# Performance work log

Measured on AMD Instinct MI355X. Metric: run time of the kernel, lower is better.

Reference implementation:

```python
import jax, jax.numpy as jnp
import numpy as np

NEG = -1.0e9


def setup_inputs() -> dict:
    key = jax.random.key(0)
    ks = jax.random.split(key, 8)
    B, L, D = 4, 2048, 1024
    s = 1.0 / np.sqrt(D)
    return {
        "x": jax.random.normal(ks[0], (B, L, D), dtype=jnp.float32),
        "Wq": jax.random.normal(ks[1], (D, D), dtype=jnp.float32) * s,
        "bq": jax.random.normal(ks[2], (D,), dtype=jnp.float32) * 0.02,
        "Wk": jax.random.normal(ks[3], (D, D), dtype=jnp.float32) * s,
        "bk": jax.random.normal(ks[4], (D,), dtype=jnp.float32) * 0.02,
        "Wv": jax.random.normal(ks[5], (D, D), dtype=jnp.float32) * s,
        "bv": jax.random.normal(ks[6], (D,), dtype=jnp.float32) * 0.02,
        "lengths": jax.random.randint(ks[7], (B,), 1, 2048, dtype=jnp.int32),
    }


def reference(x, Wq, bq, Wk, bk, Wv, bv, lengths):
    # x: [B, L, D]; single-head self-attention with causal + length additive masks
    B, L, D = x.shape
    q = x @ Wq + bq  # [B, L, D]
    k = x @ Wk + bk
    v = x @ Wv + bv
    scale = 1.0 / jnp.sqrt(jnp.asarray(D, dtype=x.dtype))
    att = jnp.einsum("bid,bjd->bij", q, k) * scale  # [B, L, L]
    idx = jnp.arange(L)
    causal = jnp.where(idx[None, :] > idx[:, None], NEG, 0.0).astype(x.dtype)  # [L, L]
    # length mask: NEG where j >= len[b] or i >= len[b]
    invalid = (idx[None, :] >= lengths[:, None])  # [B, L]
    lenmask = jnp.where(invalid[:, :, None] | invalid[:, None, :], NEG, 0.0).astype(x.dtype)
    att = att + causal[None, :, :] + lenmask
    att = jax.nn.softmax(att, axis=-1)
    return jnp.einsum("bij,bjd->bid", att, v)
```

## Files before the change

### kernel.cpp

```cpp
#include <hip/hip_runtime.h>

#define NEGV (-1.0e9f)

typedef __bf16 bf16_t;
typedef __bf16 bf16x8 __attribute__((ext_vector_type(8)));
typedef __bf16 bf16x4 __attribute__((ext_vector_type(4)));
typedef float  f32x4  __attribute__((ext_vector_type(4)));

__device__ __forceinline__ void gld16(const void* g, void* l) {
    __builtin_amdgcn_global_load_lds(
        (const __attribute__((address_space(1))) void*)g,
        (__attribute__((address_space(3))) void*)l, 16, 0, 0);
}


#define MMR(AF, IB)                                                                        \
    acc[IB][0] = __builtin_amdgcn_mfma_f32_16x16x32_bf16(AF, b0, acc[IB][0], 0, 0, 0);     \
    acc[IB][1] = __builtin_amdgcn_mfma_f32_16x16x32_bf16(AF, b1, acc[IB][1], 0, 0, 0);     \
    acc[IB][2] = __builtin_amdgcn_mfma_f32_16x16x32_bf16(AF, b2, acc[IB][2], 0, 0, 0);     \
    acc[IB][3] = __builtin_amdgcn_mfma_f32_16x16x32_bf16(AF, b3, acc[IB][3], 0, 0, 0)

__device__ __forceinline__ void ml256x256(
    const bf16_t* __restrict__ A, const bf16_t* __restrict__ B,
    int ldA, int ldB, int nkt, char* smem, int tid, f32x4 acc[8][4])
{
    const int w = tid >> 6, lane = tid & 63;
    const int wm = w & 1, wn = w >> 1;
    const int l16 = lane & 15, quad = lane >> 4;

    const int g0 = 2 * (tid >> 3) + ((tid >> 2) & 1);
    const int c0 = ((tid & 3) ^ ((tid >> 3) & 3)) * 8;
    const bf16_t* pa0 = A + (size_t)g0 * ldA + c0;
    const bf16_t* pa1 = pa0 + (size_t)128 * ldA;
    const bf16_t* pb0 = B + (size_t)g0 * ldB + c0;
    const bf16_t* pb1 = pb0 + (size_t)128 * ldB;
    char* const stA = smem + (w << 10);
    char* const stB = smem + 16384 + (w << 10);

    const int rowo = (l16 >> 1) * 128 + (l16 & 1) * 64 + ((quad ^ ((l16 >> 1) & 3)) << 4);
    const char* rdA = smem + (wm << 13) + rowo;
    const char* rdB = smem + 16384 + (wn << 12) + rowo;

#define STG6(BO) do { gld16(pa0, stA + (BO)); gld16(pa1, stA + (BO) + 8192);   \
                      gld16(pb0, stB + (BO)); gld16(pb1, stB + (BO) + 8192);   \
                      pa0 += 32; pa1 += 32; pb0 += 32; pb1 += 32; } while (0)

    STG6(0);
    if (nkt > 1) {
        STG6(32768);
        asm volatile("s_waitcnt vmcnt(4)" ::: "memory");
    } else {
        asm volatile("s_waitcnt vmcnt(0)" ::: "memory");
    }
    __builtin_amdgcn_s_barrier();

    int ro = 0, so = 65536;
    for (int kt = 0; kt < nkt; ++kt) {
        const char* ra = rdA + ro;
        const char* rb = rdB + ro;
        bf16x8 a0 = *(const bf16x8*)(ra);
        bf16x8 a1 = *(const bf16x8*)(ra + 1024);
        bf16x8 a2 = *(const bf16x8*)(ra + 2048);
        bf16x8 a3 = *(const bf16x8*)(ra + 3072);
        bf16x8 b0 = *(const bf16x8*)(rb);
        bf16x8 b1 = *(const bf16x8*)(rb + 1024);
        bf16x8 b2 = *(const bf16x8*)(rb + 2048);
        bf16x8 b3 = *(const bf16x8*)(rb + 3072);
        bf16x8 a4 = *(const bf16x8*)(ra + 4096);
        bf16x8 a5 = *(const bf16x8*)(ra + 5120);
        bf16x8 a6 = *(const bf16x8*)(ra + 6144);
        bf16x8 a7 = *(const bf16x8*)(ra + 7168);
        const bool st = (kt + 2) < nkt;
        if (st) STG6(so);
        asm volatile("s_waitcnt lgkmcnt(4)" ::: "memory");
        __builtin_amdgcn_sched_barrier(0);
        __builtin_amdgcn_s_setprio(1);
        MMR(a0, 0); MMR(a1, 1); MMR(a2, 2); MMR(a3, 3);
        __builtin_amdgcn_s_setprio(0);
        asm volatile("s_waitcnt lgkmcnt(0)" ::: "memory");
        __builtin_amdgcn_sched_barrier(0);
        __builtin_amdgcn_s_setprio(1);
        MMR(a4, 4); MMR(a5, 5); MMR(a6, 6); MMR(a7, 7);
        __builtin_amdgcn_s_setprio(0);
        if (st) asm volatile("s_waitcnt vmcnt(4)" ::: "memory");
        else    asm volatile("s_waitcnt vmcnt(0)" ::: "memory");
        __builtin_amdgcn_s_barrier();
        ro = (ro == 65536) ? 0 : (ro + 32768);
        so = (so == 65536) ? 0 : (so + 32768);
    }
#undef STG6
}

__device__ __forceinline__ void ml256x128(
    const bf16_t* __restrict__ A, const bf16_t* __restrict__ B,
    int ldA, int ldB, int nkt, char* smem, int tid, f32x4 acc[4][4])
{
    const int w = tid >> 6, lane = tid & 63;
    const int wm = w & 3, wn = w >> 2;
    const int l16 = lane & 15, quad = lane >> 4;

    const int g0 = 2 * (tid >> 3) + ((tid >> 2) & 1);
    const int c0 = ((tid & 3) ^ ((tid >> 3) & 3)) * 8;
    const bf16_t* pa0 = A + (size_t)g0 * ldA + c0;
    const bf16_t* pa1 = pa0 + (size_t)128 * ldA;
    const bf16_t* pb0 = B + (size_t)g0 * ldB + c0;
    char* const stA = smem + (w << 10);
    char* const stB = smem + 16384 + (w << 10);

    const int rowo = (l16 >> 1) * 128 + (l16 & 1) * 64 + ((quad ^ ((l16 >> 1) & 3)) << 4);
    const char* rdA = smem + (wm << 12) + rowo;
    const char* rdB = smem + 16384 + (wn << 12) + rowo;

#define STG3(BO) do { gld16(pa0, stA + (BO)); gld16(pa1, stA + (BO) + 8192);   \
                      gld16(pb0, stB + (BO));                                  \
                      pa0 += 32; pa1 += 32; pb0 += 32; } while (0)

    STG3(0);
    if (nkt > 1) {
        STG3(24576);
        asm volatile("s_waitcnt vmcnt(3)" ::: "memory");
    } else {
        asm volatile("s_waitcnt vmcnt(0)" ::: "memory");
    }
    __builtin_amdgcn_s_barrier();

    int ro = 0, so = 49152;
    for (int kt = 0; kt < nkt; ++kt) {
        const char* ra = rdA + ro;
        const char* rb = rdB + ro;
        bf16x8 a0 = *(const bf16x8*)(ra);
        bf16x8 a1 = *(const bf16x8*)(ra + 1024);
        bf16x8 a2 = *(const bf16x8*)(ra + 2048);
        bf16x8 a3 = *(const bf16x8*)(ra + 3072);
        bf16x8 b0 = *(const bf16x8*)(rb);
        bf16x8 b1 = *(const bf16x8*)(rb + 1024);
        bf16x8 b2 = *(const bf16x8*)(rb + 2048);
        bf16x8 b3 = *(const bf16x8*)(rb + 3072);
        const bool st = (kt + 2) < nkt;
        if (st) STG3(so);
        asm volatile("s_waitcnt lgkmcnt(0)" ::: "memory");
        __builtin_amdgcn_sched_barrier(0);
        __builtin_amdgcn_s_setprio(1);
        MMR(a0, 0); MMR(a1, 1); MMR(a2, 2); MMR(a3, 3);
        __builtin_amdgcn_s_setprio(0);
        if (st) asm volatile("s_waitcnt vmcnt(3)" ::: "memory");
        else    asm volatile("s_waitcnt vmcnt(0)" ::: "memory");
        __builtin_amdgcn_s_barrier();
        ro = (ro == 49152) ? 0 : (ro + 24576);
        so = (so == 49152) ? 0 : (so + 24576);
    }
#undef STG3
}

__global__ __launch_bounds__(256)
void convert_x_kernel(const float* __restrict__ x, bf16_t* __restrict__ xb)
{
    const size_t i = ((size_t)blockIdx.x * 256 + threadIdx.x) * 8;
    float4 a = *(const float4*)&x[i];
    float4 b = *(const float4*)&x[i + 4];
    bf16x8 o;
    o[0] = (bf16_t)a.x; o[1] = (bf16_t)a.y; o[2] = (bf16_t)a.z; o[3] = (bf16_t)a.w;
    o[4] = (bf16_t)b.x; o[5] = (bf16_t)b.y; o[6] = (bf16_t)b.z; o[7] = (bf16_t)b.w;
    *(bf16x8*)&xb[i] = o;
}

__global__ __launch_bounds__(256)
void transpose_w_kernel(const float* __restrict__ W0, const float* __restrict__ W1,
                        const float* __restrict__ W2, bf16_t* __restrict__ WT)
{
    __shared__ float t[32][33];
    const float* W = (blockIdx.z == 0) ? W0 : (blockIdx.z == 1) ? W1 : W2;
    bf16_t* WTz = WT + (size_t)blockIdx.z * 1024 * 1024;
    const int k0 = blockIdx.y * 32, n0 = blockIdx.x * 32;
    const int r = threadIdx.x >> 3, c4 = (threadIdx.x & 7) * 4;
    float4 v = *(const float4*)&W[(size_t)(k0 + r) * 1024 + n0 + c4];
    t[r][c4 + 0] = v.x; t[r][c4 + 1] = v.y; t[r][c4 + 2] = v.z; t[r][c4 + 3] = v.w;
    __syncthreads();
    bf16x4 o;
#pragma unroll
    for (int j = 0; j < 4; ++j) o[j] = (bf16_t)t[c4 + j][r];
    *(bf16x4*)&WTz[(size_t)(n0 + r) * 1024 + k0 + c4] = o;
}

__global__ __launch_bounds__(512, 2)
void gemm_qk256(const bf16_t* __restrict__ A, const bf16_t* __restrict__ Bt,
                const float* __restrict__ bq, const float* __restrict__ bk,
                bf16_t* __restrict__ C, int N, int Kd)
{
    __shared__ __align__(16) char smem[98304];
    int bid = blockIdx.y * 8 + blockIdx.x;
    bid = (bid & 7) * 32 + (bid >> 3);
    const int n0 = (bid & 7) * 256;
    const int m0 = (bid >> 3) * 256;
    const int tid = threadIdx.x;

    f32x4 acc[8][4];
#pragma unroll
    for (int i = 0; i < 8; ++i)
#pragma unroll
        for (int j = 0; j < 4; ++j) acc[i][j] = (f32x4)(0.0f);

    ml256x256(A + (size_t)m0 * Kd, Bt + (size_t)n0 * Kd, Kd, Kd, Kd >> 5,
              smem, tid, acc);

    const int w = tid >> 6, lane = tid & 63;
    const int wm = w & 1, wn = w >> 1, quad = lane >> 4, l16 = lane & 15;
#pragma unroll
    for (int j = 0; j < 4; ++j) {
        const int col = n0 + wn * 64 + j * 16 + l16;
        const float bval = (col < 1024) ? bq[col] : bk[col - 1024];
#pragma unroll
        for (int i = 0; i < 8; ++i) {
            const int row = m0 + wm * 128 + i * 16 + quad * 4;
#pragma unroll
            for (int r = 0; r < 4; ++r)
                C[(size_t)(row + r) * N + col] = (bf16_t)(acc[i][j][r] + bval);
        }
    }
}

__global__ __launch_bounds__(512, 2)
void gemm_vt256(const bf16_t* __restrict__ WvT, const bf16_t* __restrict__ xb,
                const float* __restrict__ bv, bf16_t* __restrict__ VT,
                int N, int Kd)
{
    __shared__ __align__(16) char smem[73728];
    int bid = blockIdx.y * 64 + blockIdx.x;
    bid = (bid & 7) * 32 + (bid >> 3);
    const int m0 = (bid >> 6) * 256;
    const int n0 = (bid & 63) * 128;
    const int tid = threadIdx.x;

    f32x4 acc[4][4];
#pragma unroll
    for (int i = 0; i < 4; ++i)
#pragma unroll
        for (int j = 0; j < 4; ++j) acc[i][j] = (f32x4)(0.0f);

    ml256x128(WvT + (size_t)m0 * Kd, xb + (size_t)n0 * Kd, Kd, Kd, Kd >> 5,
              smem, tid, acc);

    const int w = tid >> 6, lane = tid & 63;
    const int wm = w & 3, wn = w >> 2, quad = lane >> 4, l16 = lane & 15;
#pragma unroll
    for (int i = 0; i < 4; ++i) {
        const int row = m0 + wm * 64 + i * 16 + quad * 4;
#pragma unroll
        for (int r = 0; r < 4; ++r) {
            const float bval = bv[row + r];
#pragma unroll
            for (int j = 0; j < 4; ++j) {
                const int col = n0 + wn * 64 + j * 16 + l16;
                VT[(size_t)(row + r) * N + col] = (bf16_t)(acc[i][j][r] + bval);
            }
        }
    }
}

__global__ __launch_bounds__(512, 2)
void scores256(const bf16_t* __restrict__ Q, const bf16_t* __restrict__ K,
               int ldq, const int* __restrict__ lengths,
               bf16_t* __restrict__ U, float2* __restrict__ stats,
               int L, int Dd, float alpha)
{
    __shared__ __align__(16) char smem[98304];
    const int b = blockIdx.z;
    const int len = lengths[b];
    int it = 0;
    while ((it + 1) * (it + 2) / 2 <= (int)blockIdx.x) ++it;
    const int jt = blockIdx.x - it * (it + 1) / 2;
    const int m0 = it * 256, n0 = jt * 256;
    const int tid = threadIdx.x;

    f32x4 acc[8][4];
#pragma unroll
    for (int i = 0; i < 8; ++i)
#pragma unroll
        for (int j = 0; j < 4; ++j) acc[i][j] = (f32x4)(0.0f);

    const bf16_t* Qb = Q + (size_t)b * L * ldq + (size_t)m0 * ldq;
    const bf16_t* Kb = K + (size_t)b * L * ldq + (size_t)n0 * ldq;
    ml256x256(Qb, Kb, ldq, ldq, Dd >> 5, smem, tid, acc);

    const int w = tid >> 6, lane = tid & 63;
    const int wm = w & 1, wn = w >> 1, quad = lane >> 4, l16 = lane & 15;
    bf16_t* Ub = U + (size_t)b * L * L;
    float2* strow = stats + (size_t)b * L * 32;
    const int chnk = (n0 >> 6) + wn;
#pragma unroll
    for (int i = 0; i < 8; ++i) {
#pragma unroll
        for (int r = 0; r < 4; ++r) {
            const int row = m0 + wm * 128 + i * 16 + quad * 4 + r;
            float sv[4];
#pragma unroll
            for (int j = 0; j < 4; ++j) {
                const int col = n0 + wn * 64 + j * 16 + l16;
                float v = acc[i][j][r] * alpha;
                if (col > row) v += NEGV;
                if (row >= len || col >= len) v += NEGV;
                sv[j] = v;
            }
            float m = fmaxf(fmaxf(sv[0], sv[1]), fmaxf(sv[2], sv[3]));
            m = fmaxf(m, __shfl_xor(m, 1, 64));
            m = fmaxf(m, __shfl_xor(m, 2, 64));
            m = fmaxf(m, __shfl_xor(m, 4, 64));
            m = fmaxf(m, __shfl_xor(m, 8, 64));
            float ssum = 0.f;
#pragma unroll
            for (int j = 0; j < 4; ++j) {
                sv[j] = __expf(sv[j] - m);
                ssum += sv[j];
            }
            ssum += __shfl_xor(ssum, 1, 64);
            ssum += __shfl_xor(ssum, 2, 64);
            ssum += __shfl_xor(ssum, 4, 64);
            ssum += __shfl_xor(ssum, 8, 64);
#pragma unroll
            for (int j = 0; j < 4; ++j)
                Ub[(size_t)row * L + n0 + wn * 64 + j * 16 + l16] = (bf16_t)sv[j];
            if (l16 == 0) strow[(size_t)row * 32 + chnk] = make_float2(m, ssum);
        }
    }
}

__global__ __launch_bounds__(256)
void sm_finalize_norm(const float2* __restrict__ stats, bf16_t* __restrict__ U,
                      int L)
{
    __shared__ float sc[32];
    const int i = blockIdx.x;
    const int bound2 = ((i >> 8) + 1) << 8;
    const int nch = bound2 >> 6;
    const size_t base = ((size_t)blockIdx.y * L + i) * 32;
    const int t = threadIdx.x;

    if (t < 32) {
        float m_c = -3.0e38f, s_c = 0.f;
        if (t < nch) { float2 st = stats[base + t]; m_c = st.x; s_c = st.y; }
        float M = m_c;
        M = fmaxf(M, __shfl_xor(M, 1, 64));
        M = fmaxf(M, __shfl_xor(M, 2, 64));
        M = fmaxf(M, __shfl_xor(M, 4, 64));
        M = fmaxf(M, __shfl_xor(M, 8, 64));
        M = fmaxf(M, __shfl_xor(M, 16, 64));
        const float e = __expf(m_c - M);
        float d = s_c * e;
        d += __shfl_xor(d, 1, 64);
        d += __shfl_xor(d, 2, 64);
        d += __shfl_xor(d, 4, 64);
        d += __shfl_xor(d, 8, 64);
        d += __shfl_xor(d, 16, 64);
        sc[t] = e / d;
    }
    __syncthreads();

    const int j8 = t * 8;
    if (j8 < bound2) {
        bf16_t* row = U + ((size_t)blockIdx.y * L + i) * L;
        bf16x8 u = *(const bf16x8*)&row[j8];
        const float c = sc[t >> 3];
        bf16x8 o;
#pragma unroll
        for (int j = 0; j < 8; ++j) o[j] = (bf16_t)((float)u[j] * c);
        *(bf16x8*)&row[j8] = o;
    }
}

__global__ __launch_bounds__(512, 2)
void pv256(const bf16_t* __restrict__ P, int ldp,
           const bf16_t* __restrict__ VT, int ldv,
           float* __restrict__ O, int L, int Dd)
{
    __shared__ __align__(16) char smem[73728];
    const int b = blockIdx.z;
    int bid = blockIdx.y * 8 + blockIdx.x;
    bid = (bid & 7) * 8 + (bid >> 3);
    const int mt = 7 - (bid >> 3);
    const int m0 = mt * 256, n0 = (bid & 7) * 128;
    const int tid = threadIdx.x;

    f32x4 acc[4][4];
#pragma unroll
    for (int i = 0; i < 4; ++i)
#pragma unroll
        for (int j = 0; j < 4; ++j) acc[i][j] = (f32x4)(0.0f);

    const int nkt = (m0 + 256) >> 5;
    const bf16_t* Pb = P + (size_t)b * L * ldp + (size_t)m0 * ldp;
    const bf16_t* Vb = VT + (size_t)b * L + (size_t)n0 * ldv;
    ml256x128(Pb, Vb, ldp, ldv, nkt, smem, tid, acc);

    float* Ob = O + (size_t)b * L * Dd;
    const int w = tid >> 6, lane = tid & 63;
    const int wm = w & 3, wn = w >> 2, quad = lane >> 4, l16 = lane & 15;
#pragma unroll
    for (int i = 0; i < 4; ++i) {
        const int row = m0 + wm * 64 + i * 16 + quad * 4;
#pragma unroll
        for (int j = 0; j < 4; ++j) {
            const int col = n0 + wn * 64 + j * 16 + l16;
#pragma unroll
            for (int r = 0; r < 4; ++r)
                Ob[(size_t)(row + r) * Dd + col] = acc[i][j][r];
        }
    }
}

extern "C" void kernel_launch(void* const* d_in, const int* in_sizes, int n_in,
                              void* d_out, int out_size, void* d_ws, size_t ws_size,
                              hipStream_t stream)
{
    const float* x  = (const float*)d_in[0];
    const float* Wq = (const float*)d_in[1];
    const float* bq = (const float*)d_in[2];
    const float* Wk = (const float*)d_in[3];
    const float* bk = (const float*)d_in[4];
    const float* Wv = (const float*)d_in[5];
    const float* bv = (const float*)d_in[6];
    const int*  len = (const int*)d_in[7];
    float* out = (float*)d_out;

    const int B = 4, L = 2048, D = 1024;
    const int M = B * L;
    const int N2 = 2 * D;

    bf16_t* xb = (bf16_t*)d_ws;
    bf16_t* WT = xb + (size_t)M * D;
    bf16_t* QK = WT + (size_t)3 * D * D;
    bf16_t* VT = QK + (size_t)M * N2;
    bf16_t* U  = VT + (size_t)D * M;
    float2* stats = (float2*)(U + (size_t)B * L * L);

    convert_x_kernel<<<(M * D) / 2048, 256, 0, stream>>>(x, xb);

    transpose_w_kernel<<<dim3(32, 32, 3), 256, 0, stream>>>(Wq, Wk, Wv, WT);

    gemm_qk256<<<dim3(8, 32), 512, 0, stream>>>(xb, WT, bq, bk, QK, N2, D);

    gemm_vt256<<<dim3(64, 4), 512, 0, stream>>>(
        WT + (size_t)2 * D * D, xb, bv, VT, M, D);

    scores256<<<dim3(36, 1, B), 512, 0, stream>>>(
        QK, QK + 1024, N2, len, U, stats, L, D, 0.03125f);

    sm_finalize_norm<<<dim3(L, B), 256, 0, stream>>>(stats, U, L);

    pv256<<<dim3(8, 8, 4), 512, 0, stream>>>(U, L, VT, M, out, L, D);
}
```

Before: 246.2 us.

## Switch all GEMM stages to 128x128 tiles with 256-thread blocks

Replaces the 256x256 and 256x128 MFMA mainloops with a single 128x128 tile mainloop using 4 waves. The QK, V-transpose, scores and PV kernels all move to this smaller tile, which raises block counts and gives finer triangular granularity for the causal score and PV work. Tile-index swizzles are adjusted to match, and the normalization bound is tightened to 128-column granularity. Smaller tiles lower data reuse per block and add more global/LDS traffic relative to MFMA work, in exchange for better load balance and occupancy.

```diff
diff --git a/kernel.cpp b/kernel.cpp
--- a/kernel.cpp
+++ b/kernel.cpp
@@ -20,9 +20,9 @@
     acc[IB][2] = __builtin_amdgcn_mfma_f32_16x16x32_bf16(AF, b2, acc[IB][2], 0, 0, 0);     \
     acc[IB][3] = __builtin_amdgcn_mfma_f32_16x16x32_bf16(AF, b3, acc[IB][3], 0, 0, 0)
 
-__device__ __forceinline__ void ml256x256(
+__device__ __forceinline__ void ml128x128(
     const bf16_t* __restrict__ A, const bf16_t* __restrict__ B,
-    int ldA, int ldB, int nkt, char* smem, int tid, f32x4 acc[8][4])
+    int ldA, int ldB, int nkt, char* smem, int tid, f32x4 acc[4][4])
 {
     const int w = tid >> 6, lane = tid & 63;
     const int wm = w & 1, wn = w >> 1;
@@ -31,100 +31,30 @@
     const int g0 = 2 * (tid >> 3) + ((tid >> 2) & 1);
     const int c0 = ((tid & 3) ^ ((tid >> 3) & 3)) * 8;
     const bf16_t* pa0 = A + (size_t)g0 * ldA + c0;
-    const bf16_t* pa1 = pa0 + (size_t)128 * ldA;
+    const bf16_t* pa1 = pa0 + (size_t)64 * ldA;
     const bf16_t* pb0 = B + (size_t)g0 * ldB + c0;
-    const bf16_t* pb1 = pb0 + (size_t)128 * ldB;
+    const bf16_t* pb1 = pb0 + (size_t)64 * ldB;
     char* const stA = smem + (w << 10);
-    char* const stB = smem + 16384 + (w << 10);
+    char* const stB = smem + 24576 + (w << 10);
 
     const int rowo = (l16 >> 1) * 128 + (l16 & 1) * 64 + ((quad ^ ((l16 >> 1) & 3)) << 4);
-    const char* rdA = smem + (wm << 13) + rowo;
-    const char* rdB = smem + 16384 + (wn << 12) + rowo;
-
-#define STG6(BO) do { gld16(pa0, stA + (BO)); gld16(pa1, stA + (BO) + 8192);   \
-                      gld16(pb0, stB + (BO)); gld16(pb1, stB + (BO) + 8192);   \
+    const char* rdA = smem + (wm << 12) + rowo;
+    const char* rdB = smem + 24576 + (wn << 12) + rowo;
+
+#define STG4(BO) do { gld16(pa0, stA + (BO)); gld16(pa1, stA + (BO) + 4096);   \
+                      gld16(pb0, stB + (BO)); gld16(pb1, stB + (BO) + 4096);   \
                       pa0 += 32; pa1 += 32; pb0 += 32; pb1 += 32; } while (0)
 
-    STG6(0);
+    STG4(0);
     if (nkt > 1) {
-        STG6(32768);
+        STG4(8192);
         asm volatile("s_waitcnt vmcnt(4)" ::: "memory");
     } else {
         asm volatile("s_waitcnt vmcnt(0)" ::: "memory");
     }
     __builtin_amdgcn_s_barrier();
 
-    int ro = 0, so = 65536;
-    for (int kt = 0; kt < nkt; ++kt) {
-        const char* ra = rdA + ro;
-        const char* rb = rdB + ro;
-        bf16x8 a0 = *(const bf16x8*)(ra);
-        bf16x8 a1 = *(const bf16x8*)(ra + 1024);
-        bf16x8 a2 = *(const bf16x8*)(ra + 2048);
-        bf16x8 a3 = *(const bf16x8*)(ra + 3072);
-        bf16x8 b0 = *(const bf16x8*)(rb);
-        bf16x8 b1 = *(const bf16x8*)(rb + 1024);
-        bf16x8 b2 = *(const bf16x8*)(rb + 2048);
-        bf16x8 b3 = *(const bf16x8*)(rb + 3072);
-        bf16x8 a4 = *(const bf16x8*)(ra + 4096);
-        bf16x8 a5 = *(const bf16x8*)(ra + 5120);
-        bf16x8 a6 = *(const bf16x8*)(ra + 6144);
-        bf16x8 a7 = *(const bf16x8*)(ra + 7168);
-        const bool st = (kt + 2) < nkt;
-        if (st) STG6(so);
-        asm volatile("s_waitcnt lgkmcnt(4)" ::: "memory");
-        __builtin_amdgcn_sched_barrier(0);
-        __builtin_amdgcn_s_setprio(1);
-        MMR(a0, 0); MMR(a1, 1); MMR(a2, 2); MMR(a3, 3);
-        __builtin_amdgcn_s_setprio(0);
-        asm volatile("s_waitcnt lgkmcnt(0)" ::: "memory");
-        __builtin_amdgcn_sched_barrier(0);
-        __builtin_amdgcn_s_setprio(1);
-        MMR(a4, 4); MMR(a5, 5); MMR(a6, 6); MMR(a7, 7);
-        __builtin_amdgcn_s_setprio(0);
-        if (st) asm volatile("s_waitcnt vmcnt(4)" ::: "memory");
-        else    asm volatile("s_waitcnt vmcnt(0)" ::: "memory");
-        __builtin_amdgcn_s_barrier();
-        ro = (ro == 65536) ? 0 : (ro + 32768);
-        so = (so == 65536) ? 0 : (so + 32768);
-    }
-#undef STG6
-}
-
-__device__ __forceinline__ void ml256x128(
-    const bf16_t* __restrict__ A, const bf16_t* __restrict__ B,
-    int ldA, int ldB, int nkt, char* smem, int tid, f32x4 acc[4][4])
-{
-    const int w = tid >> 6, lane = tid & 63;
-    const int wm = w & 3, wn = w >> 2;
-    const int l16 = lane & 15, quad = lane >> 4;
-
-    const int g0 = 2 * (tid >> 3) + ((tid >> 2) & 1);
-    const int c0 = ((tid & 3) ^ ((tid >> 3) & 3)) * 8;
-    const bf16_t* pa0 = A + (size_t)g0 * ldA + c0;
-    const bf16_t* pa1 = pa0 + (size_t)128 * ldA;
-    const bf16_t* pb0 = B + (size_t)g0 * ldB + c0;
-    char* const stA = smem + (w << 10);
-    char* const stB = smem + 16384 + (w << 10);
-
-    const int rowo = (l16 >> 1) * 128 + (l16 & 1) * 64 + ((quad ^ ((l16 >> 1) & 3)) << 4);
-    const char* rdA = smem + (wm << 12) + rowo;
-    const char* rdB = smem + 16384 + (wn << 12) + rowo;
-
-#define STG3(BO) do { gld16(pa0, stA + (BO)); gld16(pa1, stA + (BO) + 8192);   \
-                      gld16(pb0, stB + (BO));                                  \
-                      pa0 += 32; pa1 += 32; pb0 += 32; } while (0)
-
-    STG3(0);
-    if (nkt > 1) {
-        STG3(24576);
-        asm volatile("s_waitcnt vmcnt(3)" ::: "memory");
-    } else {
-        asm volatile("s_waitcnt vmcnt(0)" ::: "memory");
-    }
-    __builtin_amdgcn_s_barrier();
-
-    int ro = 0, so = 49152;
+    int ro = 0, so = 16384;
     for (int kt = 0; kt < nkt; ++kt) {
         const char* ra = rdA + ro;
         const char* rb = rdB + ro;
@@ -137,19 +67,19 @@
         bf16x8 b2 = *(const bf16x8*)(rb + 2048);
         bf16x8 b3 = *(const bf16x8*)(rb + 3072);
         const bool st = (kt + 2) < nkt;
-        if (st) STG3(so);
+        if (st) STG4(so);
         asm volatile("s_waitcnt lgkmcnt(0)" ::: "memory");
         __builtin_amdgcn_sched_barrier(0);
         __builtin_amdgcn_s_setprio(1);
         MMR(a0, 0); MMR(a1, 1); MMR(a2, 2); MMR(a3, 3);
         __builtin_amdgcn_s_setprio(0);
-        if (st) asm volatile("s_waitcnt vmcnt(3)" ::: "memory");
+        if (st) asm volatile("s_waitcnt vmcnt(4)" ::: "memory");
         else    asm volatile("s_waitcnt vmcnt(0)" ::: "memory");
         __builtin_amdgcn_s_barrier();
-        ro = (ro == 49152) ? 0 : (ro + 24576);
-        so = (so == 49152) ? 0 : (so + 24576);
-    }
-#undef STG3
+        ro = (ro == 16384) ? 0 : (ro + 8192);
+        so = (so == 16384) ? 0 : (so + 8192);
+    }
+#undef STG4
 }
 
 __global__ __launch_bounds__(256)
@@ -182,25 +112,25 @@
     *(bf16x4*)&WTz[(size_t)(n0 + r) * 1024 + k0 + c4] = o;
 }
 
-__global__ __launch_bounds__(512, 2)
-void gemm_qk256(const bf16_t* __restrict__ A, const bf16_t* __restrict__ Bt,
+__global__ __launch_bounds__(256)
+void gemm_qk128(const bf16_t* __restrict__ A, const bf16_t* __restrict__ Bt,
                 const float* __restrict__ bq, const float* __restrict__ bk,
                 bf16_t* __restrict__ C, int N, int Kd)
 {
-    __shared__ __align__(16) char smem[98304];
-    int bid = blockIdx.y * 8 + blockIdx.x;
-    bid = (bid & 7) * 32 + (bid >> 3);
-    const int n0 = (bid & 7) * 256;
-    const int m0 = (bid >> 3) * 256;
+    __shared__ __align__(16) char smem[49152];
+    int bid = blockIdx.y * 16 + blockIdx.x;
+    bid = (bid & 7) * 128 + (bid >> 3);
+    const int n0 = (bid & 15) << 7;
+    const int m0 = (bid >> 4) << 7;
     const int tid = threadIdx.x;
 
-    f32x4 acc[8][4];
-#pragma unroll
-    for (int i = 0; i < 8; ++i)
+    f32x4 acc[4][4];
+#pragma unroll
+    for (int i = 0; i < 4; ++i)
 #pragma unroll
         for (int j = 0; j < 4; ++j) acc[i][j] = (f32x4)(0.0f);
 
-    ml256x256(A + (size_t)m0 * Kd, Bt + (size_t)n0 * Kd, Kd, Kd, Kd >> 5,
+    ml128x128(A + (size_t)m0 * Kd, Bt + (size_t)n0 * Kd, Kd, Kd, Kd >> 5,
               smem, tid, acc);
 
     const int w = tid >> 6, lane = tid & 63;
@@ -210,8 +140,8 @@
         const int col = n0 + wn * 64 + j * 16 + l16;
         const float bval = (col < 1024) ? bq[col] : bk[col - 1024];
 #pragma unroll
-        for (int i = 0; i < 8; ++i) {
-            const int row = m0 + wm * 128 + i * 16 + quad * 4;
+        for (int i = 0; i < 4; ++i) {
+            const int row = m0 + wm * 64 + i * 16 + quad * 4;
 #pragma unroll
             for (int r = 0; r < 4; ++r)
                 C[(size_t)(row + r) * N + col] = (bf16_t)(acc[i][j][r] + bval);
@@ -219,16 +149,16 @@
     }
 }
 
-__global__ __launch_bounds__(512, 2)
-void gemm_vt256(const bf16_t* __restrict__ WvT, const bf16_t* __restrict__ xb,
+__global__ __launch_bounds__(256)
+void gemm_vt128(const bf16_t* __restrict__ WvT, const bf16_t* __restrict__ xb,
                 const float* __restrict__ bv, bf16_t* __restrict__ VT,
                 int N, int Kd)
 {
-    __shared__ __align__(16) char smem[73728];
+    __shared__ __align__(16) char smem[49152];
     int bid = blockIdx.y * 64 + blockIdx.x;
-    bid = (bid & 7) * 32 + (bid >> 3);
-    const int m0 = (bid >> 6) * 256;
-    const int n0 = (bid & 63) * 128;
+    bid = (bid & 7) * 64 + (bid >> 3);
+    const int m0 = (bid >> 6) << 7;
+    const int n0 = (bid & 63) << 7;
     const int tid = threadIdx.x;
 
     f32x4 acc[4][4];
@@ -237,11 +167,11 @@
 #pragma unroll
         for (int j = 0; j < 4; ++j) acc[i][j] = (f32x4)(0.0f);
 
-    ml256x128(WvT + (size_t)m0 * Kd, xb + (size_t)n0 * Kd, Kd, Kd, Kd >> 5,
+    ml128x128(WvT + (size_t)m0 * Kd, xb + (size_t)n0 * Kd, Kd, Kd, Kd >> 5,
               smem, tid, acc);
 
     const int w = tid >> 6, lane = tid & 63;
-    const int wm = w & 3, wn = w >> 2, quad = lane >> 4, l16 = lane & 15;
+    const int wm = w & 1, wn = w >> 1, quad = lane >> 4, l16 = lane & 15;
 #pragma unroll
     for (int i = 0; i < 4; ++i) {
         const int row = m0 + wm * 64 + i * 16 + quad * 4;
@@ -257,30 +187,32 @@
     }
 }
 
-__global__ __launch_bounds__(512, 2)
-void scores256(const bf16_t* __restrict__ Q, const bf16_t* __restrict__ K,
+__global__ __launch_bounds__(256)
+void scores128(const bf16_t* __restrict__ Q, const bf16_t* __restrict__ K,
                int ldq, const int* __restrict__ lengths,
                bf16_t* __restrict__ U, float2* __restrict__ stats,
                int L, int Dd, float alpha)
 {
-    __shared__ __align__(16) char smem[98304];
+    __shared__ __align__(16) char smem[49152];
     const int b = blockIdx.z;
     const int len = lengths[b];
+    int tix = (int)blockIdx.x;
+    tix = (tix & 7) * 17 + (tix >> 3);
     int it = 0;
-    while ((it + 1) * (it + 2) / 2 <= (int)blockIdx.x) ++it;
-    const int jt = blockIdx.x - it * (it + 1) / 2;
-    const int m0 = it * 256, n0 = jt * 256;
+    while ((it + 1) * (it + 2) / 2 <= tix) ++it;
+    const int jt = tix - it * (it + 1) / 2;
+    const int m0 = it << 7, n0 = jt << 7;
     const int tid = threadIdx.x;
 
-    f32x4 acc[8][4];
-#pragma unroll
-    for (int i = 0; i < 8; ++i)
+    f32x4 acc[4][4];
+#pragma unroll
+    for (int i = 0; i < 4; ++i)
 #pragma unroll
         for (int j = 0; j < 4; ++j) acc[i][j] = (f32x4)(0.0f);
 
     const bf16_t* Qb = Q + (size_t)b * L * ldq + (size_t)m0 * ldq;
     const bf16_t* Kb = K + (size_t)b * L * ldq + (size_t)n0 * ldq;
-    ml256x256(Qb, Kb, ldq, ldq, Dd >> 5, smem, tid, acc);
+    ml128x128(Qb, Kb, ldq, ldq, Dd >> 5, smem, tid, acc);
 
     const int w = tid >> 6, lane = tid & 63;
     const int wm = w & 1, wn = w >> 1, quad = lane >> 4, l16 = lane & 15;
@@ -288,10 +220,10 @@
     float2* strow = stats + (size_t)b * L * 32;
     const int chnk = (n0 >> 6) + wn;
 #pragma unroll
-    for (int i = 0; i < 8; ++i) {
+    for (int i = 0; i < 4; ++i) {
 #pragma unroll
         for (int r = 0; r < 4; ++r) {
-            const int row = m0 + wm * 128 + i * 16 + quad * 4 + r;
+            const int row = m0 + wm * 64 + i * 16 + quad * 4 + r;
             float sv[4];
 #pragma unroll
             for (int j = 0; j < 4; ++j) {
@@ -330,8 +262,8 @@
 {
     __shared__ float sc[32];
     const int i = blockIdx.x;
-    const int bound2 = ((i >> 8) + 1) << 8;
-    const int nch = bound2 >> 6;
+    const int bound = ((i >> 7) + 1) << 7;
+    const int nch = bound >> 6;
     const size_t base = ((size_t)blockIdx.y * L + i) * 32;
     const int t = threadIdx.x;
 
@@ -356,7 +288,7 @@
     __syncthreads();
 
     const int j8 = t * 8;
-    if (j8 < bound2) {
+    if (j8 < bound) {
         bf16_t* row = U + ((size_t)blockIdx.y * L + i) * L;
         bf16x8 u = *(const bf16x8*)&row[j8];
         const float c = sc[t >> 3];
@@ -367,17 +299,16 @@
     }
 }
 
-__global__ __launch_bounds__(512, 2)
-void pv256(const bf16_t* __restrict__ P, int ldp,
+__global__ __launch_bounds__(256)
+void pv128(const bf16_t* __restrict__ P, int ldp,
            const bf16_t* __restrict__ VT, int ldv,
            float* __restrict__ O, int L, int Dd)
 {
-    __shared__ __align__(16) char smem[73728];
+    __shared__ __align__(16) char smem[49152];
     const int b = blockIdx.z;
-    int bid = blockIdx.y * 8 + blockIdx.x;
-    bid = (bid & 7) * 8 + (bid >> 3);
-    const int mt = 7 - (bid >> 3);
-    const int m0 = mt * 256, n0 = (bid & 7) * 128;
+    const int bid = blockIdx.y * 8 + blockIdx.x;
+    const int mt = 15 - (bid >> 3);
+    const int m0 = mt << 7, n0 = (bid & 7) << 7;
     const int tid = threadIdx.x;
 
     f32x4 acc[4][4];
@@ -386,14 +317,14 @@
 #pragma unroll
         for (int j = 0; j < 4; ++j) acc[i][j] = (f32x4)(0.0f);
 
-    const int nkt = (m0 + 256) >> 5;
+    const int nkt = (m0 + 128) >> 5;
     const bf16_t* Pb = P + (size_t)b * L * ldp + (size_t)m0 * ldp;
     const bf16_t* Vb = VT + (size_t)b * L + (size_t)n0 * ldv;
-    ml256x128(Pb, Vb, ldp, ldv, nkt, smem, tid, acc);
+    ml128x128(Pb, Vb, ldp, ldv, nkt, smem, tid, acc);
 
     float* Ob = O + (size_t)b * L * Dd;
     const int w = tid >> 6, lane = tid & 63;
-    const int wm = w & 3, wn = w >> 2, quad = lane >> 4, l16 = lane & 15;
+    const int wm = w & 1, wn = w >> 1, quad = lane >> 4, l16 = lane & 15;
 #pragma unroll
     for (int i = 0; i < 4; ++i) {
         const int row = m0 + wm * 64 + i * 16 + quad * 4;
@@ -436,15 +367,15 @@
 
     transpose_w_kernel<<<dim3(32, 32, 3), 256, 0, stream>>>(Wq, Wk, Wv, WT);
 
-    gemm_qk256<<<dim3(8, 32), 512, 0, stream>>>(xb, WT, bq, bk, QK, N2, D);
-
-    gemm_vt256<<<dim3(64, 4), 512, 0, stream>>>(
+    gemm_qk128<<<dim3(16, 64), 256, 0, stream>>>(xb, WT, bq, bk, QK, N2, D);
+
+    gemm_vt128<<<dim3(64, 8), 256, 0, stream>>>(
         WT + (size_t)2 * D * D, xb, bv, VT, M, D);
 
-    scores256<<<dim3(36, 1, B), 512, 0, stream>>>(
+    scores128<<<dim3(136, 1, B), 256, 0, stream>>>(
         QK, QK + 1024, N2, len, U, stats, L, D, 0.03125f);
 
     sm_finalize_norm<<<dim3(L, B), 256, 0, stream>>>(stats, U, L);
 
-    pv256<<<dim3(8, 8, 4), 512, 0, stream>>>(U, L, VT, M, out, L, D);
-}
+    pv128<<<dim3(8, 16, 4), 256, 0, stream>>>(U, L, VT, M, out, L, D);
+}
```

Measured after the change: 256.3 us. 1.04x slower.
